# Kernel tuning notes

Hardware: AMD Instinct MI355X
Metric: run time of the kernel (lower is better)

Reference implementation:

```python
import jax, jax.numpy as jnp
import numpy as np

N, D, C, K, M = 32768, 512, 64, 16, 128
DEPTH = 4            # log2(K): decision-tree depth per codebook
NODES = K - 1        # 15 internal tree nodes per codebook


def _build_selection_matrix():
    # Node i of the binary tree lives at level log2(i+1) and thresholds the
    # level-l selected dimension of its codebook.
    S = np.zeros((C * NODES, C * DEPTH), dtype=np.float32)
    base = np.zeros((NODES, DEPTH), dtype=np.float32)
    for i in range(NODES):
        base[i, int(np.log2(i + 1))] = 1.0
    for c in range(C):
        S[c * NODES:(c + 1) * NODES, c * DEPTH:(c + 1) * DEPTH] = base
    return S


def _build_bit_matrix():
    # Leaf k scores +1/-1 on each of its DEPTH ancestor nodes; the true leaf
    # attains the maximal score DEPTH.
    base = np.zeros((K, NODES), dtype=np.float32)
    for k in range(K):
        for l in range(DEPTH):
            node = (1 << l) - 1 + (k >> (DEPTH - l))   # ancestor at level l
            bit = (k >> (DEPTH - 1 - l)) & 1            # right(1)/left(0)
            base[k, node] = 1.0 if bit else -1.0
    B = np.zeros((C * K, C * NODES), dtype=np.float32)
    for c in range(C):
        B[c * K:(c + 1) * K, c * NODES:(c + 1) * NODES] = base
    return B


def setup_inputs() -> dict:
    key = jax.random.key(0)
    k1, k2, k3, k4 = jax.random.split(key, 4)
    I = jax.random.normal(k1, (N, D), jnp.float32)
    T = jax.random.normal(k2, (C * NODES,), jnp.float32) * 0.1   # thresholds
    L = jax.random.normal(k3, (M, C, K), jnp.float32)            # LUT
    dims = jnp.sort(jax.random.randint(k4, (C * DEPTH,), 0, D))  # selected cols
    S = jnp.asarray(_build_selection_matrix())
    B = jnp.asarray(_build_bit_matrix())
    temp = jnp.ones((1,), jnp.float32)
    return {"I": I, "T": T, "L": L, "S": S, "B": B, "dims": dims, "temp": temp}


def reference(I, T, L, S, B, dims, temp):
    t = temp[0]
    x_sel = I[:, dims]                                  # (N, C*DEPTH) gather
    h = x_sel @ S.T - T                                 # (N, C*NODES)
    tanh_h = jnp.tanh(h / t)
    # straight-through sign: forward sign(h), backward d(tanh(h/t))
    sign_ste = jnp.sign(h) - jax.lax.stop_gradient(tanh_h) + tanh_h
    b = sign_ste @ B.T                                  # (N, C*K) leaf scores
    soft = jax.nn.softmax(b.reshape(-1, C, K) / t, axis=2)
    hard = jax.nn.one_hot(jnp.argmax(soft, axis=2), K, dtype=soft.dtype)
    # straight-through one-hot encoding E: forward hard, backward soft
    E = hard - jax.lax.stop_gradient(soft) + soft       # (N, C, K)
    return jnp.einsum("nck,mck->nm", E, L)              # LUT gather-sum readout
```

## Files before the change

kernel.cpp:

```cpp
#include <hip/hip_runtime.h>

#define N_TOTAL 32768
#define D_DIM   512
#define C_DIM   64
#define K_DIM   16
#define M_DIM   128
#define NODES_  15

typedef unsigned short u16;
typedef unsigned int   u32;
typedef unsigned long long u64;
typedef unsigned char  u8;
typedef float  f32x4   __attribute__((ext_vector_type(4)));
typedef short  short8v __attribute__((ext_vector_type(8)));

__device__ __forceinline__ u32 f2bf_bits(float f) {
    u32 u = __float_as_uint(f);
    return (u + 0x7FFFu + ((u >> 16) & 1u)) >> 16;
}

__device__ __forceinline__ void gload_lds16(const float* g, float* l) {
    __builtin_amdgcn_global_load_lds(
        (const __attribute__((address_space(1))) void*)g,
        (__attribute__((address_space(3))) void*)l, 16, 0, 0);
}

__global__ __launch_bounds__(256) void build_lbf(
    const float* __restrict__ L, u16* __restrict__ Lbf)
{
    int idx  = blockIdx.x * 256 + threadIdx.x;
    int lane = idx & 63;
    int ch   = (idx >> 6) & 31;
    int ct   = idx >> 11;
    int m  = ct * 16 + (lane & 15);
    int k0 = ch * 32 + ((lane >> 4) * 8);
    const float* src = L + (size_t)m * 1024 + k0;
    float4 a = *(const float4*)(src);
    float4 b = *(const float4*)(src + 4);
    u32 w0 = f2bf_bits(a.x) | (f2bf_bits(a.y) << 16);
    u32 w1 = f2bf_bits(a.z) | (f2bf_bits(a.w) << 16);
    u32 w2 = f2bf_bits(b.x) | (f2bf_bits(b.y) << 16);
    u32 w3 = f2bf_bits(b.z) | (f2bf_bits(b.w) << 16);
    *(uint4*)(Lbf + (size_t)idx * 8) = make_uint4(w0, w1, w2, w3);
}

__global__ __launch_bounds__(256) void mega_kernel(
    const float* __restrict__ I,
    const float* __restrict__ T,
    const int* __restrict__ dims,
    const u16* __restrict__ Lbf,
    float* __restrict__ out)
{
    __shared__ float sI[16 * D_DIM];
    __shared__ float sT[C_DIM * NODES_];
    __shared__ u8    sC2[C_DIM * 16 * 4];

    const int tid  = threadIdx.x;
    const int lane = tid & 63;
    const int wv   = tid >> 6;
    const int rowBase = blockIdx.x * 64;

    const int4 dml = ((const int4*)dims)[lane];

    {
        const float* src = I + (size_t)(rowBase + wv * 4) * D_DIM;
        float* dst = sI + wv * 4 * D_DIM;
        #pragma unroll
        for (int i = 0; i < 8; ++i)
            gload_lds16(src + i * 256 + lane * 4, dst + i * 256);
    }
    for (int j = tid; j < C_DIM * NODES_; j += 256) sT[j] = T[j];
    __syncthreads();

    const float* tc = sT + lane * NODES_;

    #pragma unroll
    for (int ci = 0; ci < 4; ++ci) {
        if (ci) asm volatile("s_waitcnt vmcnt(0)" ::: "memory");
        u32 cp = 0;
        #pragma unroll
        for (int rr = 0; rr < 4; ++rr) {
            const float* v = sI + (wv * 4 + rr) * D_DIM;
            float x0 = v[dml.x], x1 = v[dml.y], x2 = v[dml.z], x3 = v[dml.w];
            int node = 0, k = 0;
            int b0 = (x0 - tc[0] > 0.0f) ? 1 : 0;
            k = b0; node = 1 + b0;
            int b1 = (x1 - tc[node] > 0.0f) ? 1 : 0;
            k = (k << 1) | b1; node = (node << 1) + 1 + b1;
            int b2 = (x2 - tc[node] > 0.0f) ? 1 : 0;
            k = (k << 1) | b2; node = (node << 1) + 1 + b2;
            int b3 = (x3 - tc[node] > 0.0f) ? 1 : 0;
            k = (k << 1) | b3;
            cp |= (u32)k << (4 * rr);
        }
        #pragma unroll
        for (int rr = 0; rr < 4; ++rr)
            sC2[lane * 64 + (wv * 4 + rr) * 4 + ci] = (cp >> (4 * rr)) & 15u;
        if (ci < 3) {
            const float* src = I + (size_t)(rowBase + (ci + 1) * 16 + wv * 4) * D_DIM;
            float* dst = sI + wv * 4 * D_DIM;
            #pragma unroll
            for (int i = 0; i < 8; ++i)
                gload_lds16(src + i * 256 + lane * 4, dst + i * 256);
        }
    }
    __syncthreads();

    const int l15     = lane & 15;
    const int clsLane = (lane >> 5) & 1;
    const int kb      = ((lane >> 4) & 1) * 8;

    f32x4 acc[4][2] = {};

    const u16* lb0 = Lbf + ((size_t)(wv * 2 + 0) * 32 * 64 + lane) * 8;
    const u16* lb1 = Lbf + ((size_t)(wv * 2 + 1) * 32 * 64 + lane) * 8;

    #pragma unroll 4
    for (int ch = 0; ch < 32; ++ch) {
        union { uint4 u; short8v v; } b0, b1;
        b0.u = *(const uint4*)(lb0 + (size_t)ch * 64 * 8);
        b1.u = *(const uint4*)(lb1 + (size_t)ch * 64 * 8);
        const int cls = ch * 2 + clsLane;
        const u32 codes4 = *(const u32*)(sC2 + cls * 64 + l15 * 4);
        #pragma unroll
        for (int rt = 0; rt < 4; ++rt) {
            u32 cd = (codes4 >> (8 * rt)) & 0xFFu;
            u32 tt = cd - (u32)kb;
            u64 sv = 0x3F80ull << ((tt & 3) * 16);
            union { u64 d[2]; short8v v; } a;
            a.d[0] = (tt < 4) ? sv : 0ull;
            a.d[1] = (tt >= 4 && tt < 8) ? sv : 0ull;
            acc[rt][0] = __builtin_amdgcn_mfma_f32_16x16x32_bf16(
                             a.v, b0.v, acc[rt][0], 0, 0, 0);
            acc[rt][1] = __builtin_amdgcn_mfma_f32_16x16x32_bf16(
                             a.v, b1.v, acc[rt][1], 0, 0, 0);
        }
    }

    #pragma unroll
    for (int rt = 0; rt < 4; ++rt) {
        #pragma unroll
        for (int cj = 0; cj < 2; ++cj) {
            int col = (wv * 2 + cj) * 16 + l15;
            int r0  = rowBase + rt * 16 + ((lane >> 4) << 2);
            float* o = out + (size_t)r0 * M_DIM + col;
            o[0 * M_DIM] = acc[rt][cj][0];
            o[1 * M_DIM] = acc[rt][cj][1];
            o[2 * M_DIM] = acc[rt][cj][2];
            o[3 * M_DIM] = acc[rt][cj][3];
        }
    }
}

extern "C" void kernel_launch(void* const* d_in, const int* in_sizes, int n_in,
                              void* d_out, int out_size, void* d_ws, size_t ws_size,
                              hipStream_t stream) {
    const float* I    = (const float*)d_in[0];
    const float* T    = (const float*)d_in[1];
    const float* L    = (const float*)d_in[2];
    const int*   dims = (const int*)d_in[5];

    u16* Lbf = (u16*)d_ws;

    hipLaunchKernelGGL(build_lbf, dim3(64), dim3(256), 0, stream, L, Lbf);
    hipLaunchKernelGGL(mega_kernel, dim3(N_TOTAL / 64), dim3(256), 0, stream,
                       I, T, dims, Lbf, (float*)d_out);
}
```

Baseline: 120.2 us.

## Double-buffer input tile loads and pack tree codes into padded word stores

Result: faster. 117.7 us (-2.1%).

```diff
diff --git a/kernel.cpp b/kernel.cpp
--- a/kernel.cpp
+++ b/kernel.cpp
@@ -13,6 +13,8 @@
 typedef unsigned char  u8;
 typedef float  f32x4   __attribute__((ext_vector_type(4)));
 typedef short  short8v __attribute__((ext_vector_type(8)));
+
+#define WAIT_VM(N) asm volatile("s_waitcnt vmcnt(" #N ")" ::: "memory")
 
 __device__ __forceinline__ u32 f2bf_bits(float f) {
     u32 u = __float_as_uint(f);
@@ -51,9 +53,9 @@
     const u16* __restrict__ Lbf,
     float* __restrict__ out)
 {
-    __shared__ float sI[16 * D_DIM];
+    __shared__ float sI[2 * 16 * D_DIM];
     __shared__ float sT[C_DIM * NODES_];
-    __shared__ u8    sC2[C_DIM * 16 * 4];
+    __shared__ u8    sC2[C_DIM * 68];
 
     const int tid  = threadIdx.x;
     const int lane = tid & 63;
@@ -62,25 +64,21 @@
 
     const int4 dml = ((const int4*)dims)[lane];
 
-    {
-        const float* src = I + (size_t)(rowBase + wv * 4) * D_DIM;
-        float* dst = sI + wv * 4 * D_DIM;
+    auto issue = [&](int ci, int buf) {
+        const float* src = I + (size_t)(rowBase + ci * 16 + wv * 4) * D_DIM;
+        float* dst = sI + buf * 16 * D_DIM + wv * 4 * D_DIM;
         #pragma unroll
         for (int i = 0; i < 8; ++i)
             gload_lds16(src + i * 256 + lane * 4, dst + i * 256);
-    }
-    for (int j = tid; j < C_DIM * NODES_; j += 256) sT[j] = T[j];
-    __syncthreads();
+    };
 
+    u32 c4[4] = {0u, 0u, 0u, 0u};
     const float* tc = sT + lane * NODES_;
 
-    #pragma unroll
-    for (int ci = 0; ci < 4; ++ci) {
-        if (ci) asm volatile("s_waitcnt vmcnt(0)" ::: "memory");
-        u32 cp = 0;
+    auto descend = [&](int buf, int ci) {
         #pragma unroll
         for (int rr = 0; rr < 4; ++rr) {
-            const float* v = sI + (wv * 4 + rr) * D_DIM;
+            const float* v = sI + buf * 16 * D_DIM + (wv * 4 + rr) * D_DIM;
             float x0 = v[dml.x], x1 = v[dml.y], x2 = v[dml.z], x3 = v[dml.w];
             int node = 0, k = 0;
             int b0 = (x0 - tc[0] > 0.0f) ? 1 : 0;
@@ -91,19 +89,28 @@
             k = (k << 1) | b2; node = (node << 1) + 1 + b2;
             int b3 = (x3 - tc[node] > 0.0f) ? 1 : 0;
             k = (k << 1) | b3;
-            cp |= (u32)k << (4 * rr);
+            c4[rr] |= (u32)k << (8 * ci);
         }
-        #pragma unroll
-        for (int rr = 0; rr < 4; ++rr)
-            sC2[lane * 64 + (wv * 4 + rr) * 4 + ci] = (cp >> (4 * rr)) & 15u;
-        if (ci < 3) {
-            const float* src = I + (size_t)(rowBase + (ci + 1) * 16 + wv * 4) * D_DIM;
-            float* dst = sI + wv * 4 * D_DIM;
-            #pragma unroll
-            for (int i = 0; i < 8; ++i)
-                gload_lds16(src + i * 256 + lane * 4, dst + i * 256);
-        }
-    }
+    };
+
+    issue(0, 0);
+    for (int j = tid; j < C_DIM * NODES_; j += 256) sT[j] = T[j];
+    __syncthreads();
+    issue(1, 1);
+
+    descend(0, 0);
+    issue(2, 0);
+    WAIT_VM(8);
+    descend(1, 1);
+    issue(3, 1);
+    WAIT_VM(8);
+    descend(0, 2);
+    WAIT_VM(0);
+    descend(1, 3);
+
+    #pragma unroll
+    for (int rr = 0; rr < 4; ++rr)
+        *(u32*)(sC2 + lane * 68 + (wv * 4 + rr) * 4) = c4[rr];
     __syncthreads();
 
     const int l15     = lane & 15;
@@ -121,7 +128,7 @@
         b0.u = *(const uint4*)(lb0 + (size_t)ch * 64 * 8);
         b1.u = *(const uint4*)(lb1 + (size_t)ch * 64 * 8);
         const int cls = ch * 2 + clsLane;
-        const u32 codes4 = *(const u32*)(sC2 + cls * 64 + l15 * 4);
+        const u32 codes4 = *(const u32*)(sC2 + cls * 68 + l15 * 4);
         #pragma unroll
         for (int rt = 0; rt < 4; ++rt) {
             u32 cd = (codes4 >> (8 * rt)) & 0xFFu;
```
